# Optimization experiments

Hardware: AMD Instinct MI355X
Metric: run time of the kernel (lower is better)

Reference implementation:

```python
import jax, jax.numpy as jnp
import numpy as np
import math

B, N, D, KA, H = 8, 1024, 512, 16, 8
QD = D // 4
HD = D // H


def qsplit(x):
    q = x.shape[-1] // 4
    return x[..., :q], x[..., q:2*q], x[..., 2*q:3*q], x[..., 3*q:]


def hprod(p, q):
    pr, pi, pj, pk = qsplit(p)
    qr, qi, qj, qk = qsplit(q)
    return jnp.concatenate([
        pr*qr - pi*qi - pj*qj - pk*qk,
        pr*qi + pi*qr + pj*qk - pk*qj,
        pr*qj - pi*qk + pj*qr + pk*qi,
        pr*qk + pi*qj - pj*qi + pk*qr,
    ], axis=-1)


def qconj(x):
    r, i, j, k = qsplit(x)
    return jnp.concatenate([r, -i, -j, -k], axis=-1)


def qlin(x, w, b):
    # w: [4, qo, qi] -> Hamilton block matrix [4qo, 4qi]
    r, i, j, k = w[0], w[1], w[2], w[3]
    W = jnp.concatenate([
        jnp.concatenate([r, -i, -j, -k], axis=1),
        jnp.concatenate([i,  r, -k,  j], axis=1),
        jnp.concatenate([j,  k,  r, -i], axis=1),
        jnp.concatenate([k, -j,  i,  r], axis=1),
    ], axis=0)
    return x @ W.T + b


def qln(x, gamma, beta):
    # per-component LayerNorm over Q; gamma/beta: [4, Q]
    qd = x.shape[-1] // 4
    xs = x.reshape(x.shape[:-1] + (4, qd))
    m = xs.mean(-1, keepdims=True)
    v = xs.var(-1, keepdims=True)
    y = (xs - m) / jnp.sqrt(v + 1e-5) * gamma + beta
    return y.reshape(x.shape)


def setup_inputs():
    key = jax.random.key(0)
    ks = jax.random.split(key, 20)
    lim = math.sqrt(6.0 / (2 * QD))  # xavier for [QD, QD]
    def qw(k):
        return jax.random.uniform(k, (4, QD, QD), minval=-lim, maxval=lim)
    return {
        'q': jax.random.normal(ks[0], (B, N, D), dtype=jnp.float32),
        'spike': jax.random.uniform(ks[1], (B, N), dtype=jnp.float32),
        'mask': jnp.ones((B, N), dtype=jnp.float32),
        'theta_logit': jnp.float32(0.0),
        'w_prim': qw(ks[2]), 'b_prim': jnp.zeros((D,), jnp.float32),
        'anchors': jax.random.normal(ks[3], (KA, D)) * 0.5,
        'log_sigma': jnp.zeros((KA,), jnp.float32),
        'w_aggr': qw(ks[4]), 'b_aggr': jnp.zeros((D,), jnp.float32),
        'w_q': qw(ks[5]), 'b_q': jnp.zeros((D,), jnp.float32),
        'w_k': qw(ks[6]), 'b_k': jnp.zeros((D,), jnp.float32),
        'w_v': qw(ks[7]), 'b_v': jnp.zeros((D,), jnp.float32),
        'w_o': qw(ks[8]), 'b_o': jnp.zeros((D,), jnp.float32),
        'ln_gamma': jnp.ones((4, QD), jnp.float32),
        'ln_beta': jnp.zeros((4, QD), jnp.float32),
    }


def reference(q, spike, mask, theta_logit, w_prim, b_prim, anchors, log_sigma,
              w_aggr, b_aggr, w_q, b_q, w_k, b_k, w_v, b_v, w_o, b_o,
              ln_gamma, ln_beta):
    b, n, d = q.shape
    qd = d // 4
    # --- SpikeQuaternionRotation: rotate toward K-axis by theta = theta_max*spike ---
    theta_max = (jnp.pi / 2) * jax.nn.sigmoid(theta_logit)
    theta = theta_max * spike                      # [B, N]
    c = jnp.cos(theta)[..., None]
    s = jnp.sin(theta)[..., None]
    z = jnp.zeros_like(c)
    rot = jnp.concatenate([
        jnp.broadcast_to(c, (b, n, qd)),
        jnp.broadcast_to(z, (b, n, qd)),
        jnp.broadcast_to(z, (b, n, qd)),
        jnp.broadcast_to(s, (b, n, qd)),
    ], axis=-1)
    q_rot = hprod(rot, q)                          # [B, N, D]

    # --- PrimaryLayer: per-cell quaternion transform ---
    msg_p = qlin(q_rot, w_prim, b_prim)

    # --- QuaternionAnchorLayer ---
    a_conj = qconj(anchors)                        # [KA, D]
    prod = hprod(q_rot[:, None, :, :], a_conj[None, :, None, :])  # [B, KA, N, D]
    dist = jnp.sum(prod * prod, axis=-1)           # [B, KA, N]
    sigma_sq = jnp.maximum(jnp.exp(log_sigma) ** 2, 1e-6)
    incid = jnp.exp(-dist / sigma_sq[None, :, None]) * mask[:, None, :]
    denom = jnp.maximum(incid.sum(-1, keepdims=True), 1e-6)
    h = jnp.einsum('bkn,bnd->bkd', incid, q_rot) / denom  # [B, KA, D]
    h = qlin(h, w_aggr, b_aggr)

    # --- QuaternionMHA(query=q_rot, key=h, value=h), no mask ---
    Qh = qlin(q_rot, w_q, b_q).reshape(b, n, H, HD)
    Kh = qlin(h, w_k, b_k).reshape(b, KA, H, HD)
    Vh = qlin(h, w_v, b_v).reshape(b, KA, H, HD)
    scores = jnp.einsum('bqhd,bkhd->bhqk', Qh, Kh) / jnp.sqrt(jnp.float32(HD))
    attn = jax.nn.softmax(scores, axis=-1)
    out = jnp.einsum('bhqk,bkhd->bqhd', attn, Vh).reshape(b, n, d)
    msg_a = qlin(out, w_o, b_o)

    # --- residual + per-component LayerNorm ---
    return qln(q + msg_p + msg_a, ln_gamma, ln_beta)
```

## Files before the change

kernel.cpp:

```cpp
#include <hip/hip_runtime.h>
#include <hip/hip_bf16.h>

typedef __hip_bfloat16 bf16;
typedef __attribute__((ext_vector_type(8))) short bf16x8;
typedef __attribute__((ext_vector_type(4))) float f32x4;

__device__ __forceinline__ float bflo(unsigned u) { return __uint_as_float(u << 16); }
__device__ __forceinline__ float bfhi(unsigned u) { return __uint_as_float(u & 0xffff0000u); }
__device__ __forceinline__ bool probe_f32(const void* mask) {
  return *(const unsigned*)mask == 0x3F800000u;
}
__device__ __forceinline__ float ldin(const void* p, size_t i, bool f32) {
  return f32 ? ((const float*)p)[i] : (float)((const bf16*)p)[i];
}

__global__ __launch_bounds__(256) void prologue(
    const void* w0, const void* w1, const void* w2, const void* w3,
    const void* w4, const void* w5,
    const void* b0, const void* b1, const void* b2, const void* b3,
    const void* b4, const void* b5, const void* g, const void* be,
    const void* q, const void* spike, const void* theta_logit, const void* mask,
    bf16* __restrict__ Wall, float* __restrict__ biasF,
    bf16* __restrict__ q_rot, float* __restrict__ qn) {
  bool f32 = probe_f32(mask);
  int blk = blockIdx.x, t = threadIdx.x;
  if (blk < 1536) {
    const int compT[4][4] = {{0,1,2,3},{1,0,3,2},{2,3,0,1},{3,2,1,0}};
    const float signT[4][4] = {{1.f,-1.f,-1.f,-1.f},{1.f,1.f,-1.f,1.f},{1.f,1.f,1.f,-1.f},{1.f,-1.f,1.f,1.f}};
    int E = blk * 1024 + t * 4;
    int wi = E >> 18;
    const void* src = wi == 0 ? w0 : wi == 1 ? w1 : wi == 2 ? w2 : wi == 3 ? w3 : wi == 4 ? w4 : w5;
    bf16 ov[4];
    #pragma unroll
    for (int j = 0; j < 4; ++j) {
      int e = (E + j) & 262143;
      int o = e >> 9, kk = e & 511;
      int ro = o >> 7, a = o & 127, co = kk >> 7, b2 = kk & 127;
      ov[j] = (bf16)(ldin(src, compT[ro][co] * 16384 + a * 128 + b2, f32) * signT[ro][co]);
    }
    *(uint2*)(Wall + E) = *(const uint2*)ov;
  } else if (blk < 1544) {
    int b = blk - 1536;
    const void* src = b == 0 ? b0 : b == 1 ? b1 : b == 2 ? b2 : b == 3 ? b3
                    : b == 4 ? b4 : b == 5 ? b5 : b == 6 ? g : be;
    biasF[b * 512 + t] = ldin(src, t, f32);
    biasF[b * 512 + 256 + t] = ldin(src, 256 + t, f32);
  } else {
    int row = (blk - 1544) * 2 + (t >> 7);
    int l = t & 127;
    float tl = ldin(theta_logit, 0, f32);
    float tmax = 1.5707963267948966f / (1.0f + __expf(-tl));
    float th = tmax * ldin(spike, row, f32);
    float c = cosf(th), s = sinf(th);
    size_t base = (size_t)row * 512;
    float a = ldin(q, base + l, f32), b = ldin(q, base + 128 + l, f32);
    float cc = ldin(q, base + 256 + l, f32), d = ldin(q, base + 384 + l, f32);
    float r0 = c * a - s * d;
    float r1 = c * b - s * cc;
    float r2 = c * cc + s * b;
    float r3 = c * d + s * a;
    bf16* orow = q_rot + base;
    orow[l] = (bf16)r0; orow[128 + l] = (bf16)r1; orow[256 + l] = (bf16)r2; orow[384 + l] = (bf16)r3;
    qn[(size_t)row * 128 + l] = r0 * r0 + r1 * r1 + r2 * r2 + r3 * r3;
  }
}

__device__ __forceinline__ void stage_B64(const bf16* __restrict__ Bw, int n0, char* Bs, int t) {
  int r = t & 63, cb = (t >> 6) * 16;
  const bf16* src = Bw + (size_t)(n0 + r) * 512;
  #pragma unroll
  for (int i = 0; i < 16; ++i) {
    int c = cb + i;
    int off = (c >> 2) * 4096 + (r >> 4) * 1024 + (((c & 3) * 16 + (r & 15)) * 16);
    *(uint4*)(Bs + off) = *(const uint4*)(src + c * 8);
  }
}

__global__ __launch_bounds__(256, 2) void gemm_dist(
    const bf16* __restrict__ A, const bf16* __restrict__ Bw,
    const float* __restrict__ bias0, const float* __restrict__ bias1,
    bf16* __restrict__ MQ,
    const float* __restrict__ qn, const void* anchors, const void* lsig,
    const void* mask, float* __restrict__ h_part, float* __restrict__ pd_part) {
  __shared__ char smem[77952];
  const int t = threadIdx.x;
  if (blockIdx.x >= 128) {
    char* Bs = smem;
    const int g = blockIdx.x - 128;
    const int wave = t >> 6, lane = t & 63;
    const int quad = lane >> 4, l16 = lane & 15;
    const int m0 = (g & 31) * 256, n0 = (g >> 5) * 64;
    stage_B64(Bw, n0, Bs, t);
    __syncthreads();
    const int mbase = m0 + wave * 64;
    f32x4 acc[4][4] = {};
    bf16x8 areg[2][4], breg[2][4];
    #pragma unroll
    for (int mt = 0; mt < 4; ++mt)
      areg[0][mt] = *(const bf16x8*)(A + (size_t)(mbase + mt * 16 + l16) * 512 + quad * 8);
    #pragma unroll
    for (int nt = 0; nt < 4; ++nt)
      breg[0][nt] = *(const bf16x8*)(Bs + nt * 1024 + lane * 16);
    #pragma unroll
    for (int kk = 0; kk < 16; ++kk) {
      const int cur = kk & 1, nxt = cur ^ 1;
      if (kk < 15) {
        const int k2 = (kk + 1) * 32;
        #pragma unroll
        for (int mt = 0; mt < 4; ++mt)
          areg[nxt][mt] = *(const bf16x8*)(A + (size_t)(mbase + mt * 16 + l16) * 512 + k2 + quad * 8);
        #pragma unroll
        for (int nt = 0; nt < 4; ++nt)
          breg[nxt][nt] = *(const bf16x8*)(Bs + (kk + 1) * 4096 + nt * 1024 + lane * 16);
      }
      #pragma unroll
      for (int mt = 0; mt < 4; ++mt)
        #pragma unroll
        for (int nt = 0; nt < 4; ++nt)
          acc[mt][nt] = __builtin_amdgcn_mfma_f32_16x16x32_bf16(areg[cur][mt], breg[cur][nt],
                                                                acc[mt][nt], 0, 0, 0);
    }
    #pragma unroll
    for (int nt = 0; nt < 4; ++nt) {
      int col = n0 + nt * 16 + l16;
      float bv = col < 512 ? bias0[col] : bias1[col - 512];
      #pragma unroll
      for (int mt = 0; mt < 4; ++mt) {
        int rb = mbase + mt * 16 + quad * 4;
        #pragma unroll
        for (int r = 0; r < 4; ++r)
          MQ[(size_t)(rb + r) * 1024 + col] = (bf16)(acc[mt][nt][r] + bv);
      }
    }
  } else {
    bool f32 = probe_f32(mask);
    bf16*  qr   = (bf16*)smem;
    float* an   = (float*)(smem + 65536);
    float* sInc = (float*)(smem + 73728);
    float* rs   = (float*)(smem + 77824);
    float* pd   = (float*)(smem + 77888);
    int bb = blockIdx.x;
    int b = bb >> 4, nc = bb & 15;
    {
      const uint4* src = (const uint4*)((const bf16*)A + ((size_t)b * 1024 + nc * 64) * 512);
      uint4* dst = (uint4*)qr;
      #pragma unroll
      for (int i = 0; i < 16; ++i) dst[t + i * 256] = src[t + i * 256];
    }
    for (int i = t; i < 2048; i += 256) {
      int k = i >> 7, l = i & 127;
      float a0 = ldin(anchors, k * 512 + l, f32);
      float a1 = ldin(anchors, k * 512 + 128 + l, f32);
      float a2 = ldin(anchors, k * 512 + 256 + l, f32);
      float a3 = ldin(anchors, k * 512 + 384 + l, f32);
      an[i] = a0 * a0 + a1 * a1 + a2 * a2 + a3 * a3;
    }
    if (t < 16) {
      float ls = ldin(lsig, t, f32);
      float ssq = __expf(ls); ssq = fmaxf(ssq * ssq, 1e-6f);
      rs[t] = -1.0f / ssq;
      pd[t] = 0.0f;
    }
    __syncthreads();
    {
      int rl = t >> 2, part = t & 3;
      int n = nc * 64 + rl;
      const float* qrow = qn + ((size_t)b * 1024 + n) * 128 + part * 32;
      f32x4 q4[8];
      #pragma unroll
      for (int i = 0; i < 8; ++i) q4[i] = *(const f32x4*)(qrow + i * 4);
      float sc[16] = {};
      #pragma unroll
      for (int i = 0; i < 8; ++i) {
        #pragma unroll
        for (int k = 0; k < 16; ++k) {
          f32x4 av = *(const f32x4*)(an + k * 128 + part * 32 + i * 4);
          sc[k] += q4[i][0] * av[0] + q4[i][1] * av[1] + q4[i][2] * av[2] + q4[i][3] * av[3];
        }
      }
      #pragma unroll
      for (int k = 0; k < 16; ++k) {
        sc[k] += __shfl_xor(sc[k], 1, 64);
        sc[k] += __shfl_xor(sc[k], 2, 64);
      }
      if (part == 0) {
        float mval = ldin(mask, b * 1024 + n, f32);
        #pragma unroll
        for (int k = 0; k < 16; ++k) {
          float inc = __expf(sc[k] * rs[k]) * mval;
          sInc[k * 64 + rl] = inc;
          atomicAdd(&pd[k], inc);
        }
      }
    }
    __syncthreads();
    {
      float acc0[16] = {}, acc1[16] = {};
      for (int nn = 0; nn < 64; ++nn) {
        float v0 = (float)qr[nn * 512 + t];
        float v1 = (float)qr[nn * 512 + 256 + t];
        #pragma unroll
        for (int k = 0; k < 16; ++k) {
          float p = sInc[k * 64 + nn];
          acc0[k] += p * v0;
          acc1[k] += p * v1;
        }
      }
      #pragma unroll
      for (int k = 0; k < 16; ++k) {
        size_t base = ((size_t)(b * 16 + k) * 16 + nc) * 512;
        h_part[base + t] = acc0[k];
        h_part[base + 256 + t] = acc1[k];
      }
    }
    if (t < 16) pd_part[((size_t)(b * 16 + t)) * 16 + nc] = pd[t];
  }
}

__global__ __launch_bounds__(256, 2) void gemm2(
    const bf16* __restrict__ A, const bf16* __restrict__ Bw,
    const float* __restrict__ biasO, bf16* __restrict__ msg_a) {
  __shared__ char Bs[65536];
  const int t = threadIdx.x;
  const int wave = t >> 6, lane = t & 63;
  const int quad = lane >> 4, l16 = lane & 15;
  const int m0 = blockIdx.x * 128, n0 = blockIdx.y * 64;
  stage_B64(Bw, n0, Bs, t);
  __syncthreads();
  const int mbase = m0 + wave * 32;
  f32x4 acc[2][4] = {};
  bf16x8 areg[2][2], breg[2][4];
  #pragma unroll
  for (int mt = 0; mt < 2; ++mt)
    areg[0][mt] = *(const bf16x8*)(A + (size_t)(mbase + mt * 16 + l16) * 512 + quad * 8);
  #pragma unroll
  for (int nt = 0; nt < 4; ++nt)
    breg[0][nt] = *(const bf16x8*)(Bs + nt * 1024 + lane * 16);
  #pragma unroll
  for (int kk = 0; kk < 16; ++kk) {
    const int cur = kk & 1, nxt = cur ^ 1;
    if (kk < 15) {
      const int k2 = (kk + 1) * 32;
      #pragma unroll
      for (int mt = 0; mt < 2; ++mt)
        areg[nxt][mt] = *(const bf16x8*)(A + (size_t)(mbase + mt * 16 + l16) * 512 + k2 + quad * 8);
      #pragma unroll
      for (int nt = 0; nt < 4; ++nt)
        breg[nxt][nt] = *(const bf16x8*)(Bs + (kk + 1) * 4096 + nt * 1024 + lane * 16);
    }
    #pragma unroll
    for (int mt = 0; mt < 2; ++mt)
      #pragma unroll
      for (int nt = 0; nt < 4; ++nt)
        acc[mt][nt] = __builtin_amdgcn_mfma_f32_16x16x32_bf16(areg[cur][mt], breg[cur][nt],
                                                              acc[mt][nt], 0, 0, 0);
  }
  #pragma unroll
  for (int nt = 0; nt < 4; ++nt) {
    int col = n0 + nt * 16 + l16;
    float bv = biasO[col];
    #pragma unroll
    for (int mt = 0; mt < 2; ++mt) {
      int rb = mbase + mt * 16 + quad * 4;
      #pragma unroll
      for (int r = 0; r < 4; ++r)
        msg_a[(size_t)(rb + r) * 512 + col] = (bf16)(acc[mt][nt][r] + bv);
    }
  }
}

__global__ __launch_bounds__(256) void qlin_akv(
    const float* __restrict__ h_part, const float* __restrict__ pd_part,
    const bf16* __restrict__ Wa, const float* __restrict__ ba,
    const bf16* __restrict__ Wk, const float* __restrict__ bk,
    const bf16* __restrict__ Wv, const float* __restrict__ bv,
    float* __restrict__ Kh, float* __restrict__ Vh) {
  __shared__ float xs[512];
  __shared__ float ys[512];
  int row = blockIdx.x, half = blockIdx.y;
  int t = threadIdx.x;
  float dsum = 0.0f;
  #pragma unroll
  for (int nc = 0; nc < 16; ++nc) dsum += pd_part[row * 16 + nc];
  float dinv = 1.0f / fmaxf(dsum, 1e-6f);
  #pragma unroll
  for (int j = 0; j < 2; ++j) {
    int d = j * 256 + t;
    float hv = 0.0f;
    #pragma unroll
    for (int nc = 0; nc < 16; ++nc) hv += h_part[(size_t)row * 8192 + nc * 512 + d];
    xs[d] = hv * dinv;
  }
  __syncthreads();
  #pragma unroll
  for (int j = 0; j < 2; ++j) {
    int o = j * 256 + t;
    const uint4* wr = (const uint4*)(Wa + (size_t)o * 512);
    float acc = ba[o];
    #pragma unroll 4
    for (int c = 0; c < 64; ++c) {
      uint4 u = wr[c];
      const float* xp = xs + c * 8;
      acc += xp[0] * bflo(u.x) + xp[1] * bfhi(u.x)
           + xp[2] * bflo(u.y) + xp[3] * bfhi(u.y)
           + xp[4] * bflo(u.z) + xp[5] * bfhi(u.z)
           + xp[6] * bflo(u.w) + xp[7] * bfhi(u.w);
    }
    ys[o] = acc;
  }
  __syncthreads();
  {
    int o = half * 256 + t;
    const uint4* wk = (const uint4*)(Wk + (size_t)o * 512);
    const uint4* wv = (const uint4*)(Wv + (size_t)o * 512);
    float ak = bk[o], av = bv[o];
    #pragma unroll 2
    for (int c = 0; c < 64; ++c) {
      uint4 uk = wk[c], uv = wv[c];
      const float* xp = ys + c * 8;
      ak += xp[0] * bflo(uk.x) + xp[1] * bfhi(uk.x)
          + xp[2] * bflo(uk.y) + xp[3] * bfhi(uk.y)
          + xp[4] * bflo(uk.z) + xp[5] * bfhi(uk.z)
          + xp[6] * bflo(uk.w) + xp[7] * bfhi(uk.w);
      av += xp[0] * bflo(uv.x) + xp[1] * bfhi(uv.x)
          + xp[2] * bflo(uv.y) + xp[3] * bfhi(uv.y)
          + xp[4] * bflo(uv.z) + xp[5] * bfhi(uv.z)
          + xp[6] * bflo(uv.w) + xp[7] * bfhi(uv.w);
    }
    Kh[(size_t)row * 512 + o] = ak;
    Vh[(size_t)row * 512 + o] = av;
  }
}

__global__ __launch_bounds__(256) void attn_v3(
    const bf16* __restrict__ MQ, const float* __restrict__ Kh_g,
    const float* __restrict__ Vh_g, bf16* __restrict__ attn_o) {
  __shared__ float KV[8 * 1092];
  __shared__ float P[16 * 132];
  const int t = threadIdx.x;
  const int rowbase = blockIdx.x * 16;
  const int b = rowbase >> 10;
  for (int i = t; i < 8192; i += 256) {
    int k = i >> 9, d = i & 511, h = d >> 6, dd = d & 63;
    KV[h * 1092 + k * 68 + dd] = Kh_g[(size_t)b * 8192 + i];
  }
  __syncthreads();
  {
    const int r = t >> 4, h = (t >> 1) & 7, hf = t & 1;
    const int grow = rowbase + r;
    const uint4* qp = (const uint4*)(MQ + (size_t)grow * 1024 + 512 + h * 64 + hf * 32);
    float q[32];
    #pragma unroll
    for (int i = 0; i < 4; ++i) {
      uint4 u = qp[i];
      q[i * 8 + 0] = bflo(u.x); q[i * 8 + 1] = bfhi(u.x);
      q[i * 8 + 2] = bflo(u.y); q[i * 8 + 3] = bfhi(u.y);
      q[i * 8 + 4] = bflo(u.z); q[i * 8 + 5] = bfhi(u.z);
      q[i * 8 + 6] = bflo(u.w); q[i * 8 + 7] = bfhi(u.w);
    }
    float sc[16];
    #pragma unroll
    for (int k = 0; k < 16; ++k) {
      float s = 0.0f;
      #pragma unroll
      for (int d4 = 0; d4 < 8; ++d4) {
        f32x4 kv = *(const f32x4*)(KV + h * 1092 + k * 68 + hf * 32 + d4 * 4);
        s += q[d4 * 4 + 0] * kv[0] + q[d4 * 4 + 1] * kv[1]
           + q[d4 * 4 + 2] * kv[2] + q[d4 * 4 + 3] * kv[3];
      }
      sc[k] = s;
    }
    #pragma unroll
    for (int k = 0; k < 16; ++k) sc[k] += __shfl_xor(sc[k], 1, 64);
    if (hf == 0) {
      #pragma unroll
      for (int k = 0; k < 16; ++k) sc[k] *= 0.125f;
      float m = sc[0];
      #pragma unroll
      for (int k = 1; k < 16; ++k) m = fmaxf(m, sc[k]);
      float ssum = 0.0f;
      #pragma unroll
      for (int k = 0; k < 16; ++k) { sc[k] = __expf(sc[k] - m); ssum += sc[k]; }
      float inv = 1.0f / ssum;
      #pragma unroll
      for (int k = 0; k < 16; ++k) P[r * 132 + h * 16 + k] = sc[k] * inv;
    }
  }
  __syncthreads();
  for (int i = t; i < 8192; i += 256) {
    int k = i >> 9, d = i & 511, h = d >> 6, dd = d & 63;
    KV[h * 1092 + k * 68 + dd] = Vh_g[(size_t)b * 8192 + i];
  }
  __syncthreads();
  {
    const int r = t >> 4, dg = t & 15;
    #pragma unroll
    for (int h = 0; h < 8; ++h) {
      float a0 = 0, a1 = 0, a2 = 0, a3 = 0;
      #pragma unroll
      for (int k = 0; k < 16; ++k) {
        float p = P[r * 132 + h * 16 + k];
        f32x4 va = *(const f32x4*)(KV + h * 1092 + k * 68 + dg * 4);
        a0 += p * va[0]; a1 += p * va[1]; a2 += p * va[2]; a3 += p * va[3];
      }
      bf16 ov[4] = {(bf16)a0, (bf16)a1, (bf16)a2, (bf16)a3};
      *(uint2*)(attn_o + (size_t)(rowbase + r) * 512 + h * 64 + dg * 4) = *(const uint2*)ov;
    }
  }
}

__global__ __launch_bounds__(256) void ln_v2(
    const void* q, const void* mask, const bf16* __restrict__ MQ,
    const bf16* __restrict__ msg_a, const float* __restrict__ gamF, void* out) {
  bool f32 = probe_f32(mask);
  int t = threadIdx.x;
  int row = blockIdx.x * 2 + (t >> 7);
  int l = t & 127;
  int e0 = l * 4;
  float x[4];
  {
    uint2 um = *(const uint2*)(MQ + (size_t)row * 1024 + e0);
    uint2 ua = *(const uint2*)(msg_a + (size_t)row * 512 + e0);
    float qv[4];
    if (f32) {
      f32x4 qq = *(const f32x4*)((const float*)q + (size_t)row * 512 + e0);
      qv[0] = qq[0]; qv[1] = qq[1]; qv[2] = qq[2]; qv[3] = qq[3];
    } else {
      uint2 uq = *(const uint2*)((const bf16*)q + (size_t)row * 512 + e0);
      qv[0] = bflo(uq.x); qv[1] = bfhi(uq.x); qv[2] = bflo(uq.y); qv[3] = bfhi(uq.y);
    }
    x[0] = qv[0] + bflo(um.x) + bflo(ua.x);
    x[1] = qv[1] + bfhi(um.x) + bfhi(ua.x);
    x[2] = qv[2] + bflo(um.y) + bflo(ua.y);
    x[3] = qv[3] + bfhi(um.y) + bfhi(ua.y);
  }
  float s = x[0] + x[1] + x[2] + x[3];
  float s2 = x[0] * x[0] + x[1] * x[1] + x[2] * x[2] + x[3] * x[3];
  #pragma unroll
  for (int off = 1; off <= 16; off <<= 1) {
    s  += __shfl_xor(s, off, 64);
    s2 += __shfl_xor(s2, off, 64);
  }
  float m = s * (1.0f / 128.0f);
  float rinv = rsqrtf(s2 * (1.0f / 128.0f) - m * m + 1e-5f);
  f32x4 ga = *(const f32x4*)(gamF + e0);
  f32x4 be = *(const f32x4*)(gamF + 512 + e0);
  float y[4];
  #pragma unroll
  for (int j = 0; j < 4; ++j) y[j] = (x[j] - m) * rinv * ga[j] + be[j];
  if (f32) {
    f32x4 ov = {y[0], y[1], y[2], y[3]};
    *(f32x4*)((float*)out + (size_t)row * 512 + e0) = ov;
  } else {
    bf16 ov[4] = {(bf16)y[0], (bf16)y[1], (bf16)y[2], (bf16)y[3]};
    *(uint2*)((bf16*)out + (size_t)row * 512 + e0) = *(const uint2*)ov;
  }
}

extern "C" void kernel_launch(void* const* d_in, const int* in_sizes, int n_in,
                              void* d_out, int out_size, void* d_ws, size_t ws_size,
                              hipStream_t stream) {
  (void)in_sizes; (void)n_in; (void)out_size; (void)ws_size;
  const void* q      = d_in[0];
  const void* spike  = d_in[1];
  const void* mask   = d_in[2];
  const void* tl     = d_in[3];
  const void* w_prim = d_in[4];
  const void* b_prim = d_in[5];
  const void* anchors= d_in[6];
  const void* lsig   = d_in[7];
  const void* w_aggr = d_in[8];
  const void* b_aggr = d_in[9];
  const void* w_q    = d_in[10];
  const void* b_q    = d_in[11];
  const void* w_k    = d_in[12];
  const void* b_k    = d_in[13];
  const void* w_v    = d_in[14];
  const void* b_v    = d_in[15];
  const void* w_o    = d_in[16];
  const void* b_o    = d_in[17];
  const void* gam    = d_in[18];
  const void* bet    = d_in[19];

  char* ws = (char*)d_ws;
  bf16*  Wall   = (bf16*)(ws + 0);
  bf16*  q_rot  = (bf16*)(ws + 3145728);
  float* qn     = (float*)(ws + 11534336);
  bf16*  MQ     = (bf16*)(ws + 15728640);
  float* h_part = (float*)(ws + 32505856);
  float* pd_part= (float*)(ws + 36700160);
  float* Kh     = (float*)(ws + 36708352);
  float* Vh     = (float*)(ws + 36970496);
  bf16*  attn_o = (bf16*)(ws + 37232640);
  bf16*  msg_a  = (bf16*)(ws + 45621248);
  float* biasF  = (float*)(ws + 54009856);

  prologue<<<5640, 256, 0, stream>>>(w_prim, w_q, w_o, w_aggr, w_k, w_v,
                                     b_prim, b_q, b_o, b_aggr, b_k, b_v, gam, bet,
                                     q, spike, tl, mask, Wall, biasF, q_rot, qn);
  gemm_dist<<<640, 256, 0, stream>>>(q_rot, Wall, biasF + 0, biasF + 512, MQ,
                                     qn, anchors, lsig, mask, h_part, pd_part);
  qlin_akv<<<dim3(128, 2), 256, 0, stream>>>(h_part, pd_part,
                                             Wall + 3 * 262144, biasF + 1536,
                                             Wall + 4 * 262144, biasF + 2048,
                                             Wall + 5 * 262144, biasF + 2560, Kh, Vh);
  attn_v3<<<512, 256, 0, stream>>>(MQ, Kh, Vh, attn_o);
  gemm2<<<dim3(64, 8), 256, 0, stream>>>(attn_o, Wall + 2 * 262144, biasF + 1024, msg_a);
  ln_v2<<<4096, 256, 0, stream>>>(q, mask, MQ, msg_a, biasF + 3072, d_out);
}
```

Measured before the change: 213.6 us.

## Pre-swizzle weights into MFMA tile layout and fuse attention, output GEMM, LayerNorm

The prologue now writes the Hamilton weight matrices straight into the tiled LDS/MFMA layout, so staging B becomes a plain contiguous copy and qlin_akv reads the tiled layout through a helper. The attention kernel is merged with the output projection GEMM and the residual LayerNorm. Attention output goes to LDS as bf16 and is multiplied against W_o, which each wave reads directly from global memory. This removes the attn_o and msg_a round trips through global memory and two kernel launches. In exchange, each block does a 16x512x512 GEMM with B fetched from global memory rather than shared memory, and holds more registers per thread.

```diff
diff --git a/kernel.cpp b/kernel.cpp
--- a/kernel.cpp
+++ b/kernel.cpp
@@ -14,11 +14,12 @@
   return f32 ? ((const float*)p)[i] : (float)((const bf16*)p)[i];
 }
 
+
 __global__ __launch_bounds__(256) void prologue(
     const void* w0, const void* w1, const void* w2, const void* w3,
     const void* w4, const void* w5,
     const void* b0, const void* b1, const void* b2, const void* b3,
-    const void* b4, const void* b5, const void* g, const void* be,
+    const void* b4, const void* b5, const void* g_, const void* be,
     const void* q, const void* spike, const void* theta_logit, const void* mask,
     bf16* __restrict__ Wall, float* __restrict__ biasF,
     bf16* __restrict__ q_rot, float* __restrict__ qn) {
@@ -28,21 +29,28 @@
     const int compT[4][4] = {{0,1,2,3},{1,0,3,2},{2,3,0,1},{3,2,1,0}};
     const float signT[4][4] = {{1.f,-1.f,-1.f,-1.f},{1.f,1.f,-1.f,1.f},{1.f,1.f,1.f,-1.f},{1.f,-1.f,1.f,1.f}};
     int E = blk * 1024 + t * 4;
-    int wi = E >> 18;
+    int g = E >> 9;
+    int wi = g >> 9;
+    int o = g & 511;
+    int k0 = E & 511;
     const void* src = wi == 0 ? w0 : wi == 1 ? w1 : wi == 2 ? w2 : wi == 3 ? w3 : wi == 4 ? w4 : w5;
+    int ro = o >> 7, a = o & 127, co = k0 >> 7;
+    int comp = compT[ro][co];
+    float sgn = signT[ro][co];
     bf16 ov[4];
     #pragma unroll
     for (int j = 0; j < 4; ++j) {
-      int e = (E + j) & 262143;
-      int o = e >> 9, kk = e & 511;
-      int ro = o >> 7, a = o & 127, co = kk >> 7, b2 = kk & 127;
-      ov[j] = (bf16)(ldin(src, compT[ro][co] * 16384 + a * 128 + b2, f32) * signT[ro][co]);
-    }
-    *(uint2*)(Wall + E) = *(const uint2*)ov;
+      int b2 = (k0 & 127) + j;
+      ov[j] = (bf16)(ldin(src, comp * 16384 + a * 128 + b2, f32) * sgn);
+    }
+    int r = g & 63, c = k0 >> 3;
+    size_t off = (size_t)(g >> 6) * 65536 + (size_t)((c >> 2) * 4096 + (r >> 4) * 1024
+               + ((c & 3) * 16 + (r & 15)) * 16 + (k0 & 7) * 2);
+    *(uint2*)((char*)Wall + off) = *(const uint2*)ov;
   } else if (blk < 1544) {
     int b = blk - 1536;
     const void* src = b == 0 ? b0 : b == 1 ? b1 : b == 2 ? b2 : b == 3 ? b3
-                    : b == 4 ? b4 : b == 5 ? b5 : b == 6 ? g : be;
+                    : b == 4 ? b4 : b == 5 ? b5 : b == 6 ? g_ : be;
     biasF[b * 512 + t] = ldin(src, t, f32);
     biasF[b * 512 + 256 + t] = ldin(src, 256 + t, f32);
   } else {
@@ -66,14 +74,10 @@
 }
 
 __device__ __forceinline__ void stage_B64(const bf16* __restrict__ Bw, int n0, char* Bs, int t) {
-  int r = t & 63, cb = (t >> 6) * 16;
-  const bf16* src = Bw + (size_t)(n0 + r) * 512;
-  #pragma unroll
-  for (int i = 0; i < 16; ++i) {
-    int c = cb + i;
-    int off = (c >> 2) * 4096 + (r >> 4) * 1024 + (((c & 3) * 16 + (r & 15)) * 16);
-    *(uint4*)(Bs + off) = *(const uint4*)(src + c * 8);
-  }
+  const char* src = (const char*)Bw + (size_t)(n0 >> 6) * 65536;
+  #pragma unroll
+  for (int i = 0; i < 16; ++i)
+    *(uint4*)(Bs + t * 16 + i * 4096) = *(const uint4*)(src + t * 16 + i * 4096);
 }
 
 __global__ __launch_bounds__(256, 2) void gemm_dist(
@@ -217,126 +221,72 @@
   }
 }
 
-__global__ __launch_bounds__(256, 2) void gemm2(
-    const bf16* __restrict__ A, const bf16* __restrict__ Bw,
-    const float* __restrict__ biasO, bf16* __restrict__ msg_a) {
-  __shared__ char Bs[65536];
-  const int t = threadIdx.x;
-  const int wave = t >> 6, lane = t & 63;
-  const int quad = lane >> 4, l16 = lane & 15;
-  const int m0 = blockIdx.x * 128, n0 = blockIdx.y * 64;
-  stage_B64(Bw, n0, Bs, t);
-  __syncthreads();
-  const int mbase = m0 + wave * 32;
-  f32x4 acc[2][4] = {};
-  bf16x8 areg[2][2], breg[2][4];
-  #pragma unroll
-  for (int mt = 0; mt < 2; ++mt)
-    areg[0][mt] = *(const bf16x8*)(A + (size_t)(mbase + mt * 16 + l16) * 512 + quad * 8);
-  #pragma unroll
-  for (int nt = 0; nt < 4; ++nt)
-    breg[0][nt] = *(const bf16x8*)(Bs + nt * 1024 + lane * 16);
-  #pragma unroll
-  for (int kk = 0; kk < 16; ++kk) {
-    const int cur = kk & 1, nxt = cur ^ 1;
-    if (kk < 15) {
-      const int k2 = (kk + 1) * 32;
-      #pragma unroll
-      for (int mt = 0; mt < 2; ++mt)
-        areg[nxt][mt] = *(const bf16x8*)(A + (size_t)(mbase + mt * 16 + l16) * 512 + k2 + quad * 8);
-      #pragma unroll
-      for (int nt = 0; nt < 4; ++nt)
-        breg[nxt][nt] = *(const bf16x8*)(Bs + (kk + 1) * 4096 + nt * 1024 + lane * 16);
-    }
-    #pragma unroll
-    for (int mt = 0; mt < 2; ++mt)
-      #pragma unroll
-      for (int nt = 0; nt < 4; ++nt)
-        acc[mt][nt] = __builtin_amdgcn_mfma_f32_16x16x32_bf16(areg[cur][mt], breg[cur][nt],
-                                                              acc[mt][nt], 0, 0, 0);
-  }
-  #pragma unroll
-  for (int nt = 0; nt < 4; ++nt) {
-    int col = n0 + nt * 16 + l16;
-    float bv = biasO[col];
-    #pragma unroll
-    for (int mt = 0; mt < 2; ++mt) {
-      int rb = mbase + mt * 16 + quad * 4;
-      #pragma unroll
-      for (int r = 0; r < 4; ++r)
-        msg_a[(size_t)(rb + r) * 512 + col] = (bf16)(acc[mt][nt][r] + bv);
-    }
-  }
-}
-
-__global__ __launch_bounds__(256) void qlin_akv(
-    const float* __restrict__ h_part, const float* __restrict__ pd_part,
-    const bf16* __restrict__ Wa, const float* __restrict__ ba,
-    const bf16* __restrict__ Wk, const float* __restrict__ bk,
-    const bf16* __restrict__ Wv, const float* __restrict__ bv,
-    float* __restrict__ Kh, float* __restrict__ Vh) {
-  __shared__ float xs[512];
-  __shared__ float ys[512];
-  int row = blockIdx.x, half = blockIdx.y;
-  int t = threadIdx.x;
-  float dsum = 0.0f;
-  #pragma unroll
-  for (int nc = 0; nc < 16; ++nc) dsum += pd_part[row * 16 + nc];
-  float dinv = 1.0f / fmaxf(dsum, 1e-6f);
-  #pragma unroll
-  for (int j = 0; j < 2; ++j) {
-    int d = j * 256 + t;
-    float hv = 0.0f;
-    #pragma unroll
-    for (int nc = 0; nc < 16; ++nc) hv += h_part[(size_t)row * 8192 + nc * 512 + d];
-    xs[d] = hv * dinv;
-  }
-  __syncthreads();
-  #pragma unroll
-  for (int j = 0; j < 2; ++j) {
-    int o = j * 256 + t;
-    const uint4* wr = (const uint4*)(Wa + (size_t)o * 512);
-    float acc = ba[o];
-    #pragma unroll 4
-    for (int c = 0; c < 64; ++c) {
-      uint4 u = wr[c];
-      const float* xp = xs + c * 8;
+__device__ __forceinline__ float dotW(const char* WallB, int gRow, const float* xp512) {
+  const char* p = WallB + (size_t)(gRow >> 6) * 65536
+                + (size_t)(((gRow >> 4) & 3) * 1024 + (gRow & 15) * 16);
+  float acc = 0.0f;
+  #pragma unroll 4
+  for (int c4 = 0; c4 < 16; ++c4) {
+    #pragma unroll
+    for (int cl = 0; cl < 4; ++cl) {
+      uint4 u = *(const uint4*)(p + c4 * 4096 + cl * 256);
+      const float* xp = xp512 + c4 * 32 + cl * 8;
       acc += xp[0] * bflo(u.x) + xp[1] * bfhi(u.x)
            + xp[2] * bflo(u.y) + xp[3] * bfhi(u.y)
            + xp[4] * bflo(u.z) + xp[5] * bfhi(u.z)
            + xp[6] * bflo(u.w) + xp[7] * bfhi(u.w);
     }
-    ys[o] = acc;
+  }
+  return acc;
+}
+
+__global__ __launch_bounds__(256) void qlin_akv(
+    const float* __restrict__ h_part, const float* __restrict__ pd_part,
+    const bf16* __restrict__ Wall, const float* __restrict__ biasF,
+    float* __restrict__ Kh, float* __restrict__ Vh) {
+  __shared__ float xs[512];
+  __shared__ float ys[512];
+  const char* WallB = (const char*)Wall;
+  const float* ba = biasF + 1536;
+  const float* bk = biasF + 2048;
+  const float* bv = biasF + 2560;
+  int row = blockIdx.x, half = blockIdx.y;
+  int t = threadIdx.x;
+  float dsum = 0.0f;
+  #pragma unroll
+  for (int nc = 0; nc < 16; ++nc) dsum += pd_part[row * 16 + nc];
+  float dinv = 1.0f / fmaxf(dsum, 1e-6f);
+  #pragma unroll
+  for (int j = 0; j < 2; ++j) {
+    int d = j * 256 + t;
+    float hv = 0.0f;
+    #pragma unroll
+    for (int nc = 0; nc < 16; ++nc) hv += h_part[(size_t)row * 8192 + nc * 512 + d];
+    xs[d] = hv * dinv;
+  }
+  __syncthreads();
+  #pragma unroll
+  for (int j = 0; j < 2; ++j) {
+    int o = j * 256 + t;
+    ys[o] = ba[o] + dotW(WallB, 1536 + o, xs);
   }
   __syncthreads();
   {
     int o = half * 256 + t;
-    const uint4* wk = (const uint4*)(Wk + (size_t)o * 512);
-    const uint4* wv = (const uint4*)(Wv + (size_t)o * 512);
-    float ak = bk[o], av = bv[o];
-    #pragma unroll 2
-    for (int c = 0; c < 64; ++c) {
-      uint4 uk = wk[c], uv = wv[c];
-      const float* xp = ys + c * 8;
-      ak += xp[0] * bflo(uk.x) + xp[1] * bfhi(uk.x)
-          + xp[2] * bflo(uk.y) + xp[3] * bfhi(uk.y)
-          + xp[4] * bflo(uk.z) + xp[5] * bfhi(uk.z)
-          + xp[6] * bflo(uk.w) + xp[7] * bfhi(uk.w);
-      av += xp[0] * bflo(uv.x) + xp[1] * bfhi(uv.x)
-          + xp[2] * bflo(uv.y) + xp[3] * bfhi(uv.y)
-          + xp[4] * bflo(uv.z) + xp[5] * bfhi(uv.z)
-          + xp[6] * bflo(uv.w) + xp[7] * bfhi(uv.w);
-    }
+    float ak = bk[o] + dotW(WallB, 2048 + o, ys);
+    float av = bv[o] + dotW(WallB, 2560 + o, ys);
     Kh[(size_t)row * 512 + o] = ak;
     Vh[(size_t)row * 512 + o] = av;
   }
 }
 
-__global__ __launch_bounds__(256) void attn_v3(
+__global__ __launch_bounds__(256, 2) void attn_tail(
     const bf16* __restrict__ MQ, const float* __restrict__ Kh_g,
-    const float* __restrict__ Vh_g, bf16* __restrict__ attn_o) {
+    const float* __restrict__ Vh_g, const bf16* __restrict__ Wall,
+    const float* __restrict__ biasF, const void* q, const void* mask, void* out) {
   __shared__ float KV[8 * 1092];
   __shared__ float P[16 * 132];
+  const bool f32 = probe_f32(mask);
   const int t = threadIdx.x;
   const int rowbase = blockIdx.x * 16;
   const int b = rowbase >> 10;
@@ -349,14 +299,14 @@
     const int r = t >> 4, h = (t >> 1) & 7, hf = t & 1;
     const int grow = rowbase + r;
     const uint4* qp = (const uint4*)(MQ + (size_t)grow * 1024 + 512 + h * 64 + hf * 32);
-    float q[32];
+    float qv[32];
     #pragma unroll
     for (int i = 0; i < 4; ++i) {
       uint4 u = qp[i];
-      q[i * 8 + 0] = bflo(u.x); q[i * 8 + 1] = bfhi(u.x);
-      q[i * 8 + 2] = bflo(u.y); q[i * 8 + 3] = bfhi(u.y);
-      q[i * 8 + 4] = bflo(u.z); q[i * 8 + 5] = bfhi(u.z);
-      q[i * 8 + 6] = bflo(u.w); q[i * 8 + 7] = bfhi(u.w);
+      qv[i * 8 + 0] = bflo(u.x); qv[i * 8 + 1] = bfhi(u.x);
+      qv[i * 8 + 2] = bflo(u.y); qv[i * 8 + 3] = bfhi(u.y);
+      qv[i * 8 + 4] = bflo(u.z); qv[i * 8 + 5] = bfhi(u.z);
+      qv[i * 8 + 6] = bflo(u.w); qv[i * 8 + 7] = bfhi(u.w);
     }
     float sc[16];
     #pragma unroll
@@ -365,8 +315,8 @@
       #pragma unroll
       for (int d4 = 0; d4 < 8; ++d4) {
         f32x4 kv = *(const f32x4*)(KV + h * 1092 + k * 68 + hf * 32 + d4 * 4);
-        s += q[d4 * 4 + 0] * kv[0] + q[d4 * 4 + 1] * kv[1]
-           + q[d4 * 4 + 2] * kv[2] + q[d4 * 4 + 3] * kv[3];
+        s += qv[d4 * 4 + 0] * kv[0] + qv[d4 * 4 + 1] * kv[1]
+           + qv[d4 * 4 + 2] * kv[2] + qv[d4 * 4 + 3] * kv[3];
       }
       sc[k] = s;
     }
@@ -392,6 +342,7 @@
     KV[h * 1092 + k * 68 + dd] = Vh_g[(size_t)b * 8192 + i];
   }
   __syncthreads();
+  float pv[8][4];
   {
     const int r = t >> 4, dg = t & 15;
     #pragma unroll
@@ -403,57 +354,86 @@
         f32x4 va = *(const f32x4*)(KV + h * 1092 + k * 68 + dg * 4);
         a0 += p * va[0]; a1 += p * va[1]; a2 += p * va[2]; a3 += p * va[3];
       }
-      bf16 ov[4] = {(bf16)a0, (bf16)a1, (bf16)a2, (bf16)a3};
-      *(uint2*)(attn_o + (size_t)(rowbase + r) * 512 + h * 64 + dg * 4) = *(const uint2*)ov;
-    }
-  }
-}
-
-__global__ __launch_bounds__(256) void ln_v2(
-    const void* q, const void* mask, const bf16* __restrict__ MQ,
-    const bf16* __restrict__ msg_a, const float* __restrict__ gamF, void* out) {
-  bool f32 = probe_f32(mask);
-  int t = threadIdx.x;
-  int row = blockIdx.x * 2 + (t >> 7);
-  int l = t & 127;
-  int e0 = l * 4;
-  float x[4];
+      pv[h][0] = a0; pv[h][1] = a1; pv[h][2] = a2; pv[h][3] = a3;
+    }
+  }
+  __syncthreads();
+  char* A_lds = (char*)KV;
   {
-    uint2 um = *(const uint2*)(MQ + (size_t)row * 1024 + e0);
-    uint2 ua = *(const uint2*)(msg_a + (size_t)row * 512 + e0);
-    float qv[4];
-    if (f32) {
-      f32x4 qq = *(const f32x4*)((const float*)q + (size_t)row * 512 + e0);
-      qv[0] = qq[0]; qv[1] = qq[1]; qv[2] = qq[2]; qv[3] = qq[3];
-    } else {
-      uint2 uq = *(const uint2*)((const bf16*)q + (size_t)row * 512 + e0);
-      qv[0] = bflo(uq.x); qv[1] = bfhi(uq.x); qv[2] = bflo(uq.y); qv[3] = bfhi(uq.y);
-    }
-    x[0] = qv[0] + bflo(um.x) + bflo(ua.x);
-    x[1] = qv[1] + bfhi(um.x) + bfhi(ua.x);
-    x[2] = qv[2] + bflo(um.y) + bflo(ua.y);
-    x[3] = qv[3] + bfhi(um.y) + bfhi(ua.y);
-  }
-  float s = x[0] + x[1] + x[2] + x[3];
-  float s2 = x[0] * x[0] + x[1] * x[1] + x[2] * x[2] + x[3] * x[3];
-  #pragma unroll
-  for (int off = 1; off <= 16; off <<= 1) {
-    s  += __shfl_xor(s, off, 64);
-    s2 += __shfl_xor(s2, off, 64);
-  }
-  float m = s * (1.0f / 128.0f);
-  float rinv = rsqrtf(s2 * (1.0f / 128.0f) - m * m + 1e-5f);
-  f32x4 ga = *(const f32x4*)(gamF + e0);
-  f32x4 be = *(const f32x4*)(gamF + 512 + e0);
-  float y[4];
-  #pragma unroll
-  for (int j = 0; j < 4; ++j) y[j] = (x[j] - m) * rinv * ga[j] + be[j];
-  if (f32) {
-    f32x4 ov = {y[0], y[1], y[2], y[3]};
-    *(f32x4*)((float*)out + (size_t)row * 512 + e0) = ov;
-  } else {
-    bf16 ov[4] = {(bf16)y[0], (bf16)y[1], (bf16)y[2], (bf16)y[3]};
-    *(uint2*)((bf16*)out + (size_t)row * 512 + e0) = *(const uint2*)ov;
+    const int r = t >> 4, dg = t & 15;
+    #pragma unroll
+    for (int h = 0; h < 8; ++h) {
+      int c0 = h * 64 + dg * 4;
+      int off = (c0 >> 5) * 1024 + ((c0 >> 3) & 3) * 256 + r * 16 + (c0 & 7) * 2;
+      bf16 ov[4] = {(bf16)pv[h][0], (bf16)pv[h][1], (bf16)pv[h][2], (bf16)pv[h][3]};
+      *(uint2*)(A_lds + off) = *(const uint2*)ov;
+    }
+  }
+  __syncthreads();
+  const int wave = t >> 6, lane = t & 63, quad = lane >> 4, l16 = lane & 15;
+  const char* WallB = (const char*)Wall;
+  f32x4 acc[8] = {};
+  bf16x8 breg[2][8];
+  bf16x8 areg[2];
+  areg[0] = *(const bf16x8*)(A_lds + quad * 256 + l16 * 16);
+  #pragma unroll
+  for (int nt = 0; nt < 8; ++nt) {
+    size_t cb = (size_t)(16 + wave * 2 + (nt >> 2)) * 65536;
+    breg[0][nt] = *(const bf16x8*)(WallB + cb + (nt & 3) * 1024 + lane * 16);
+  }
+  #pragma unroll
+  for (int kk = 0; kk < 16; ++kk) {
+    const int cur = kk & 1, nxt = cur ^ 1;
+    if (kk < 15) {
+      areg[nxt] = *(const bf16x8*)(A_lds + (kk + 1) * 1024 + quad * 256 + l16 * 16);
+      #pragma unroll
+      for (int nt = 0; nt < 8; ++nt) {
+        size_t cb = (size_t)(16 + wave * 2 + (nt >> 2)) * 65536;
+        breg[nxt][nt] = *(const bf16x8*)(WallB + cb + (kk + 1) * 4096 + (nt & 3) * 1024 + lane * 16);
+      }
+    }
+    #pragma unroll
+    for (int nt = 0; nt < 8; ++nt)
+      acc[nt] = __builtin_amdgcn_mfma_f32_16x16x32_bf16(areg[cur], breg[cur][nt], acc[nt], 0, 0, 0);
+  }
+  const float* biasO = biasF + 1024;
+  const float* gamF = biasF + 3072;
+  float xv[8][4];
+  float s[4] = {0, 0, 0, 0}, s2[4] = {0, 0, 0, 0};
+  #pragma unroll
+  for (int nt = 0; nt < 8; ++nt) {
+    int gcol = wave * 128 + nt * 16 + l16;
+    float bo = biasO[gcol];
+    #pragma unroll
+    for (int reg = 0; reg < 4; ++reg) {
+      int grow = rowbase + quad * 4 + reg;
+      float qv = ldin(q, (size_t)grow * 512 + gcol, f32);
+      float mp = (float)MQ[(size_t)grow * 1024 + gcol];
+      float x = qv + mp + acc[nt][reg] + bo;
+      xv[nt][reg] = x;
+      s[reg] += x; s2[reg] += x * x;
+    }
+  }
+  #pragma unroll
+  for (int reg = 0; reg < 4; ++reg) {
+    #pragma unroll
+    for (int off = 1; off <= 8; off <<= 1) {
+      s[reg]  += __shfl_xor(s[reg], off, 64);
+      s2[reg] += __shfl_xor(s2[reg], off, 64);
+    }
+  }
+  #pragma unroll
+  for (int reg = 0; reg < 4; ++reg) {
+    float m = s[reg] * (1.0f / 128.0f);
+    float rinv = rsqrtf(s2[reg] * (1.0f / 128.0f) - m * m + 1e-5f);
+    int grow = rowbase + quad * 4 + reg;
+    #pragma unroll
+    for (int nt = 0; nt < 8; ++nt) {
+      int gcol = wave * 128 + nt * 16 + l16;
+      float y = (xv[nt][reg] - m) * rinv * gamF[gcol] + gamF[512 + gcol];
+      if (f32) ((float*)out)[(size_t)grow * 512 + gcol] = y;
+      else     ((bf16*)out)[(size_t)grow * 512 + gcol] = (bf16)y;
+    }
   }
 }
 
@@ -491,20 +471,13 @@
   float* pd_part= (float*)(ws + 36700160);
   float* Kh     = (float*)(ws + 36708352);
   float* Vh     = (float*)(ws + 36970496);
-  bf16*  attn_o = (bf16*)(ws + 37232640);
-  bf16*  msg_a  = (bf16*)(ws + 45621248);
-  float* biasF  = (float*)(ws + 54009856);
+  float* biasF  = (float*)(ws + 37232640);
 
   prologue<<<5640, 256, 0, stream>>>(w_prim, w_q, w_o, w_aggr, w_k, w_v,
                                      b_prim, b_q, b_o, b_aggr, b_k, b_v, gam, bet,
                                      q, spike, tl, mask, Wall, biasF, q_rot, qn);
   gemm_dist<<<640, 256, 0, stream>>>(q_rot, Wall, biasF + 0, biasF + 512, MQ,
                                      qn, anchors, lsig, mask, h_part, pd_part);
-  qlin_akv<<<dim3(128, 2), 256, 0, stream>>>(h_part, pd_part,
-                                             Wall + 3 * 262144, biasF + 1536,
-                                             Wall + 4 * 262144, biasF + 2048,
-                                             Wall + 5 * 262144, biasF + 2560, Kh, Vh);
-  attn_v3<<<512, 256, 0, stream>>>(MQ, Kh, Vh, attn_o);
-  gemm2<<<dim3(64, 8), 256, 0, stream>>>(attn_o, Wall + 2 * 262144, biasF + 1024, msg_a);
-  ln_v2<<<4096, 256, 0, stream>>>(q, mask, MQ, msg_a, biasF + 3072, d_out);
-}
+  qlin_akv<<<dim3(128, 2), 256, 0, stream>>>(h_part, pd_part, Wall, biasF, Kh, Vh);
+  attn_tail<<<512, 256, 0, stream>>>(MQ, Kh, Vh, Wall, biasF, q, mask, d_out);
+}
```

After: 227.8 us. 6.7% more time.
